# Performance work log

Hardware: AMD Instinct MI355X
Metric: run time of the kernel (lower is better)

Reference implementation:

```python
import jax, jax.numpy as jnp
import numpy as np

B, N, F_IN, F_OUT = 32, 1024, 256, 256
K_NEIGHBORS = 64
TEMPERATURE = 1.0
LN_EPS = 1e-5


def setup_inputs() -> dict:
    key = jax.random.key(0)
    ks = jax.random.split(key, 10)
    s_in = 1.0 / np.sqrt(F_IN)
    s_out = 1.0 / np.sqrt(F_OUT)
    # learned static adjacency: 0.1 everywhere + 0.9 on diagonal (self loops)
    static_edge_weights = jnp.full((N, N), 0.1, dtype=jnp.float32) + 0.9 * jnp.eye(N, dtype=jnp.float32)
    return {
        "x": jax.random.normal(ks[0], (B, N, F_IN), dtype=jnp.float32),
        "wq": jax.random.uniform(ks[1], (F_IN, F_OUT), jnp.float32, -s_in, s_in),
        "bq": jnp.zeros((F_OUT,), jnp.float32),
        "wk": jax.random.uniform(ks[2], (F_IN, F_OUT), jnp.float32, -s_in, s_in),
        "bk": jnp.zeros((F_OUT,), jnp.float32),
        "wv": jax.random.uniform(ks[3], (F_IN, F_OUT), jnp.float32, -s_in, s_in),
        "bv": jnp.zeros((F_OUT,), jnp.float32),
        "static_edge_weights": static_edge_weights,
        "w1": jax.random.uniform(ks[4], (F_OUT, F_OUT), jnp.float32, -s_out, s_out),
        "b1": jnp.zeros((F_OUT,), jnp.float32),
        "ln_g": jnp.ones((F_OUT,), jnp.float32),
        "ln_b": jnp.zeros((F_OUT,), jnp.float32),
        "w2": jax.random.uniform(ks[5], (F_OUT, F_OUT), jnp.float32, -s_out, s_out),
        "b2": jnp.zeros((F_OUT,), jnp.float32),
    }


def reference(x, wq, bq, wk, bk, wv, bv, static_edge_weights, w1, b1, ln_g, ln_b, w2, b2):
    Bc, Nc, _ = x.shape
    q = jnp.einsum("bnf,fo->bno", x, wq) + bq
    k = jnp.einsum("bnf,fo->bno", x, wk) + bk
    v = jnp.einsum("bnf,fo->bno", x, wv) + bv
    # [B, N, N] attention scores with learned static adjacency bias
    scores = jnp.einsum("bnd,bmd->bnm", q, k) / jnp.sqrt(jnp.float32(F_OUT))
    scores = scores + static_edge_weights[None, :, :]
    # top-k sparsification along last dim
    _, topk_idx = jax.lax.top_k(scores, K_NEIGHBORS)  # [B, N, K]
    bi = jnp.arange(Bc)[:, None, None]
    ni = jnp.arange(Nc)[None, :, None]
    mask = jnp.zeros(scores.shape, dtype=bool).at[bi, ni, topk_idx].set(True)
    scores = jnp.where(mask, scores, jnp.float32(-1e9))
    attn = jax.nn.softmax(scores / TEMPERATURE, axis=-1)
    messages = jnp.einsum("bnm,bmd->bnd", attn, v)
    # out_mlp: Linear -> LayerNorm -> ReLU -> Linear
    h = jnp.einsum("bnd,de->bne", messages, w1) + b1
    mu = jnp.mean(h, axis=-1, keepdims=True)
    var = jnp.mean(jnp.square(h - mu), axis=-1, keepdims=True)
    h = (h - mu) / jnp.sqrt(var + LN_EPS) * ln_g + ln_b
    h = jax.nn.relu(h)
    h = jnp.einsum("bnd,de->bne", h, w2) + b2
    out = h + v  # residual
    return (out, attn)
```

## Files before the change

### kernel.cpp

```cpp
#include <hip/hip_runtime.h>
#include <cstdint>

#define NB 32
#define NNODES 1024
#define DD 256
#define KNB 64
#define MTOT (NB * NNODES)

#define INV65536 1.52587890625e-05f
#define KCELL 2.44140625e-4f

typedef _Float16 half8 __attribute__((ext_vector_type(8)));
typedef _Float16 half4 __attribute__((ext_vector_type(4)));
typedef float f32x4 __attribute__((ext_vector_type(4)));

typedef __attribute__((address_space(3))) uint32_t lds_u32;
typedef __attribute__((address_space(1))) uint32_t glb_u32;

__device__ __forceinline__ void gll16(const _Float16* g, _Float16* l) {
  __builtin_amdgcn_global_load_lds((const glb_u32*)g, (lds_u32*)l, 16, 0, 0);
}

__device__ __forceinline__ void split2(float v, _Float16& h, _Float16& l) {
  h = (_Float16)v;
  l = (_Float16)(v - (float)h);
}

__global__ __launch_bounds__(256) void prep_w(const float* __restrict__ wq,
                                              const float* __restrict__ wk,
                                              const float* __restrict__ wv,
                                              const float* __restrict__ w1,
                                              const float* __restrict__ w2,
                                              _Float16* __restrict__ WT) {
  const int idx = blockIdx.x * 256 + threadIdx.x;
  const int wsel = idx >> 16;
  const int rem = idx & 65535;
  const int k = rem >> 8, n = rem & 255;
  const float* src = (wsel == 0) ? wq : (wsel == 1) ? wk : (wsel == 2) ? wv : (wsel == 3) ? w1 : w2;
  const float v = src[rem] * 1024.0f;
  _Float16 h1, h2;
  split2(v, h1, h2);
  WT[(size_t)wsel * 131072 + n * 256 + k] = h1;
  WT[(size_t)wsel * 131072 + 65536 + n * 256 + k] = h2;
}

__global__ __launch_bounds__(256) void prep_x(const float* __restrict__ x,
                                              _Float16* __restrict__ X1,
                                              _Float16* __restrict__ X2) {
  const size_t i = ((size_t)blockIdx.x * 256 + threadIdx.x) * 8;
  const float4 a = *(const float4*)(x + i);
  const float4 bb = *(const float4*)(x + i + 4);
  const float vals[8] = {a.x, a.y, a.z, a.w, bb.x, bb.y, bb.z, bb.w};
  half8 h, l;
#pragma unroll
  for (int e = 0; e < 8; ++e) {
    _Float16 hh, ll;
    split2(vals[e] * 64.0f, hh, ll);
    h[e] = hh;
    l[e] = ll;
  }
  *(half8*)(X1 + i) = h;
  *(half8*)(X2 + i) = l;
}

#define SWZ_OFF(r, cc) ((r) * 64 + (((cc) ^ ((r)&7)) << 3))

__global__ __launch_bounds__(256) void gemm_qkv(const _Float16* __restrict__ X1,
                                                const _Float16* __restrict__ X2,
                                                const _Float16* __restrict__ WT,
                                                const float* __restrict__ bq,
                                                const float* __restrict__ bk,
                                                const float* __restrict__ bv,
                                                _Float16* __restrict__ Q1, _Float16* __restrict__ Q2,
                                                _Float16* __restrict__ K1, _Float16* __restrict__ K2,
                                                float* __restrict__ V,
                                                _Float16* __restrict__ V16) {
  __shared__ _Float16 sm[4 * 8192];
  _Float16* sA1 = sm;
  _Float16* sA2 = sm + 8192;
  _Float16* sB1 = sm + 16384;
  _Float16* sB2 = sm + 24576;

  const int tid = threadIdx.x;
  const int lane = tid & 63, w = tid >> 6;
  const int r16 = lane & 15, kg = lane >> 4;
  const int rsub = lane >> 3, csub = lane & 7;
  const int wm = (w >> 1) * 64, wn = (w & 1) * 64;

  const int id = blockIdx.x;
  const int c8 = id & 7, t = id >> 3;
  const int gy = (t / 6) * 8 + c8;
  const int j6 = t % 6;
  const int wsel = j6 >> 1;
  const int n0 = (j6 & 1) * 128;
  const int m0 = gy * 128;
  const bool full = (wsel != 2);

  const _Float16* pB1 = WT + (size_t)wsel * 131072;
  const _Float16* pB2 = pB1 + 65536;

  f32x4 acc[4][4];
#pragma unroll
  for (int i = 0; i < 4; ++i)
#pragma unroll
    for (int j = 0; j < 4; ++j) acc[i][j] = f32x4{0.f, 0.f, 0.f, 0.f};

  for (int k0 = 0; k0 < DD; k0 += 64) {
    __syncthreads();
#pragma unroll
    for (int it = 0; it < 4; ++it) {
      const int r = (w << 5) + (it << 3) + rsub;
      const int swz = ((csub ^ (r & 7)) << 3);
      const int ldso = (w << 11) + (it << 9);
      gll16(X1 + (size_t)(m0 + r) * DD + k0 + swz, sA1 + ldso);
      gll16(pB1 + (size_t)(n0 + r) * DD + k0 + swz, sB1 + ldso);
      if (full) {
        gll16(X2 + (size_t)(m0 + r) * DD + k0 + swz, sA2 + ldso);
        gll16(pB2 + (size_t)(n0 + r) * DD + k0 + swz, sB2 + ldso);
      }
    }
    __syncthreads();

#pragma unroll
    for (int s = 0; s < 2; ++s) {
      half8 aA[4], aB[4], bA[4], bB[4];
#pragma unroll
      for (int mi = 0; mi < 4; ++mi) {
        const int off = SWZ_OFF(wm + mi * 16 + r16, s * 4 + kg);
        aA[mi] = *(const half8*)(sA1 + off);
      }
#pragma unroll
      for (int nj = 0; nj < 4; ++nj) {
        const int off = SWZ_OFF(wn + nj * 16 + r16, s * 4 + kg);
        bA[nj] = *(const half8*)(sB1 + off);
      }
      if (full) {
#pragma unroll
        for (int mi = 0; mi < 4; ++mi) {
          const int off = SWZ_OFF(wm + mi * 16 + r16, s * 4 + kg);
          aB[mi] = *(const half8*)(sA2 + off);
        }
#pragma unroll
        for (int nj = 0; nj < 4; ++nj) {
          const int off = SWZ_OFF(wn + nj * 16 + r16, s * 4 + kg);
          bB[nj] = *(const half8*)(sB2 + off);
        }
      }
#pragma unroll
      for (int mi = 0; mi < 4; ++mi)
#pragma unroll
        for (int nj = 0; nj < 4; ++nj) {
          acc[mi][nj] = __builtin_amdgcn_mfma_f32_16x16x32_f16(aA[mi], bA[nj], acc[mi][nj], 0, 0, 0);
          if (full) {
            acc[mi][nj] = __builtin_amdgcn_mfma_f32_16x16x32_f16(aA[mi], bB[nj], acc[mi][nj], 0, 0, 0);
            acc[mi][nj] = __builtin_amdgcn_mfma_f32_16x16x32_f16(aB[mi], bA[nj], acc[mi][nj], 0, 0, 0);
          }
        }
    }
  }

  const float* bsel = (wsel == 0) ? bq : (wsel == 1) ? bk : bv;
  _Float16* P1 = (wsel == 0) ? Q1 : K1;
  _Float16* P2 = (wsel == 0) ? Q2 : K2;
#pragma unroll
  for (int mi = 0; mi < 4; ++mi)
#pragma unroll
    for (int nj = 0; nj < 4; ++nj) {
      const int col = n0 + wn + nj * 16 + r16;
#pragma unroll
      for (int j = 0; j < 4; ++j) {
        const int rr = m0 + wm + mi * 16 + kg * 4 + j;
        if (wsel == 2) {
          const float val = acc[mi][nj][j] * INV65536 + bsel[col];
          V[(size_t)rr * DD + col] = val;
          if (V16) V16[(size_t)rr * DD + col] = (_Float16)val;
        } else {
          const float qv = acc[mi][nj][j] * (1.0f / 1024.0f) + 64.0f * bsel[col];
          _Float16 h1, h2;
          split2(qv, h1, h2);
          P1[(size_t)rr * DD + col] = h1;
          P2[(size_t)rr * DD + col] = h2;
        }
      }
    }
}

template <int EPI>
__global__ __launch_bounds__(256) void gemm_split(const _Float16* __restrict__ A1,
                                                  const _Float16* __restrict__ A2,
                                                  const _Float16* __restrict__ B1g,
                                                  const _Float16* __restrict__ B2g,
                                                  const float* __restrict__ bias,
                                                  const float* __restrict__ resid,
                                                  float* __restrict__ C) {
  __shared__ _Float16 sm[4 * 8192];
  _Float16* sA1 = sm;
  _Float16* sA2 = sm + 8192;
  _Float16* sB1 = sm + 16384;
  _Float16* sB2 = sm + 24576;

  const int tid = threadIdx.x;
  const int lane = tid & 63, w = tid >> 6;
  const int r16 = lane & 15, kg = lane >> 4;
  const int rsub = lane >> 3, csub = lane & 7;
  const int wm = (w >> 1) * 64, wn = (w & 1) * 64;

  const int n0 = blockIdx.x * 128;
  const int m0 = blockIdx.y * 128;

  const _Float16* pB1 = B1g;
  const _Float16* pB2 = B2g;
  if (EPI == 2) {
    const size_t boff = (size_t)(m0 >> 10) * NNODES * DD;
    pB1 += boff;
    pB2 += boff;
  }

  f32x4 acc[4][4];
#pragma unroll
  for (int i = 0; i < 4; ++i)
#pragma unroll
    for (int j = 0; j < 4; ++j) acc[i][j] = f32x4{0.f, 0.f, 0.f, 0.f};

  for (int k0 = 0; k0 < DD; k0 += 64) {
    __syncthreads();
#pragma unroll
    for (int it = 0; it < 4; ++it) {
      const int r = (w << 5) + (it << 3) + rsub;
      const int swz = ((csub ^ (r & 7)) << 3);
      const int ldso = (w << 11) + (it << 9);
      gll16(A1 + (size_t)(m0 + r) * DD + k0 + swz, sA1 + ldso);
      if (EPI == 2) gll16(A2 + (size_t)(m0 + r) * DD + k0 + swz, sA2 + ldso);
      gll16(pB1 + (size_t)(n0 + r) * DD + k0 + swz, sB1 + ldso);
      gll16(pB2 + (size_t)(n0 + r) * DD + k0 + swz, sB2 + ldso);
    }
    __syncthreads();

#pragma unroll
    for (int s = 0; s < 2; ++s) {
      half8 aA[4], aB[4], bA[4], bB[4];
#pragma unroll
      for (int mi = 0; mi < 4; ++mi) {
        const int off = SWZ_OFF(wm + mi * 16 + r16, s * 4 + kg);
        aA[mi] = *(const half8*)(sA1 + off);
        if (EPI == 2) aB[mi] = *(const half8*)(sA2 + off);
      }
#pragma unroll
      for (int nj = 0; nj < 4; ++nj) {
        const int off = SWZ_OFF(wn + nj * 16 + r16, s * 4 + kg);
        bA[nj] = *(const half8*)(sB1 + off);
        bB[nj] = *(const half8*)(sB2 + off);
      }
#pragma unroll
      for (int mi = 0; mi < 4; ++mi)
#pragma unroll
        for (int nj = 0; nj < 4; ++nj) {
          acc[mi][nj] = __builtin_amdgcn_mfma_f32_16x16x32_f16(aA[mi], bA[nj], acc[mi][nj], 0, 0, 0);
          acc[mi][nj] = __builtin_amdgcn_mfma_f32_16x16x32_f16(aA[mi], bB[nj], acc[mi][nj], 0, 0, 0);
          if (EPI == 2)
            acc[mi][nj] = __builtin_amdgcn_mfma_f32_16x16x32_f16(aB[mi], bA[nj], acc[mi][nj], 0, 0, 0);
        }
    }
  }

#pragma unroll
  for (int mi = 0; mi < 4; ++mi)
#pragma unroll
    for (int nj = 0; nj < 4; ++nj) {
      const int col = n0 + wn + nj * 16 + r16;
#pragma unroll
      for (int j = 0; j < 4; ++j) {
        const int rr = m0 + wm + mi * 16 + kg * 4 + j;
        const float v = acc[mi][nj][j] * INV65536;
        if (EPI == 2) {
          const float sv = v + bias[(size_t)(rr & (NNODES - 1)) * NNODES + col];
          const float f = fminf(fmaxf((sv + 8.0f) * 4096.0f, 0.0f), 65535.0f);
          uint16_t* kbase = (uint16_t*)((char*)C + (size_t)rr * 4096 + 2048);
          kbase[col] = (uint16_t)(unsigned)f;
        } else if (EPI == 0) {
          C[(size_t)rr * DD + col] = v + bias[col];
        } else {
          C[(size_t)rr * DD + col] = v + bias[col] + resid[(size_t)rr * DD + col];
        }
      }
    }
}

template <bool USE16>
__global__ __launch_bounds__(256) void topk_softmax_msg(float* __restrict__ S,
                                                        const float* __restrict__ V,
                                                        const _Float16* __restrict__ V16,
                                                        const _Float16* __restrict__ Q1,
                                                        const _Float16* __restrict__ Q2,
                                                        const _Float16* __restrict__ K1,
                                                        const _Float16* __restrict__ K2,
                                                        const float* __restrict__ adj,
                                                        _Float16* __restrict__ M1) {
  const int tid = threadIdx.x;
  const int w = tid >> 6, lane = tid & 63;
  const int id = blockIdx.x;
  const int xcd = id & 7, t = id >> 3;
  const int b = (t >> 8) * 8 + xcd;
  const int row = b * NNODES + (t & 255) * 4 + w;
  const int m = row & (NNODES - 1);
  float* Srow = S + (size_t)row * NNODES;
  const uint16_t* krow = (const uint16_t*)((const char*)S + (size_t)row * 4096 + 2048);

  __shared__ float2 spair[4][KNB];
  __shared__ int cidxs[4][32];
  __shared__ float cex[4][32];
  __shared__ int csel[4][32];

  if (lane < KNB) spair[w][lane] = make_float2(0.0f, __int_as_float(0));

  const uint4 u0 = *(const uint4*)(krow + lane * 8);
  const uint4 u1 = *(const uint4*)(krow + 512 + lane * 8);
  int k[16];
  {
    const unsigned uu[8] = {u0.x, u0.y, u0.z, u0.w, u1.x, u1.y, u1.z, u1.w};
#pragma unroll
    for (int q = 0; q < 8; ++q) {
      k[q * 2] = (int)(uu[q] & 0xffffu);
      k[q * 2 + 1] = (int)(uu[q] >> 16);
    }
  }

  float st[16];
#pragma unroll
  for (int t2 = 0; t2 < 16; ++t2) st[t2] = fmaf((float)k[t2] + 0.5f, KCELL, -8.0f);

  int cur = 0;
#pragma unroll 1
  for (int bit = 15; bit >= 0; --bit) {
    const int cand = cur | (1 << bit);
    int cnt = 0;
#pragma unroll
    for (int t2 = 0; t2 < 16; ++t2) cnt += (int)__popcll(__ballot(k[t2] >= cand));
    if (cnt >= KNB) cur = cand;
  }

  const int kHi = cur + 2;
  const int kLo = cur - 1;

  const unsigned long long ltmask = (1ull << lane) - 1ull;
  unsigned hm = 0u, cm = 0u;
  int cpos[16];
  int nhi = 0, ncand = 0;
#pragma unroll
  for (int g = 0; g < 2; ++g) {
    bool hiv[8], cdv[8];
    unsigned long long mh[8], mc[8];
#pragma unroll
    for (int e = 0; e < 8; ++e) {
      const int t2 = g * 8 + e;
      hiv[e] = (k[t2] >= kHi);
      cdv[e] = (!hiv[e]) && (k[t2] >= kLo);
      mh[e] = __ballot(hiv[e]);
      mc[e] = __ballot(cdv[e]);
    }
    int below = 0, tot_h = 0, tot_c = 0;
#pragma unroll
    for (int e = 0; e < 8; ++e) {
      below += (int)__popcll(mc[e] & ltmask);
      tot_h += (int)__popcll(mh[e]);
      tot_c += (int)__popcll(mc[e]);
    }
    int own = 0;
#pragma unroll
    for (int e = 0; e < 8; ++e) {
      const int t2 = g * 8 + e;
      cpos[t2] = -1;
      if (hiv[e]) hm |= (1u << t2);
      if (cdv[e]) {
        cm |= (1u << t2);
        const int p = ncand + below + own;
        cpos[t2] = p;
        if (p < 32) cidxs[w][p] = g * 512 + lane * 8 + e;
        ++own;
      }
    }
    nhi += tot_h;
    ncand += tot_c;
  }
  const int need = KNB - nhi;

  unsigned selm;
  if (ncand == need) {
    selm = hm | cm;
  } else {
    const int nc = (ncand <= 32) ? ncand : 32;
    const int nd = (need <= nc) ? need : nc;
    const size_t qoff = (size_t)row * DD + lane * 4;
    const half4 q1v = *(const half4*)(Q1 + qoff);
    const half4 q2v = *(const half4*)(Q2 + qoff);
    float qf[4];
#pragma unroll
    for (int e = 0; e < 4; ++e) qf[e] = (float)q1v[e] + (float)q2v[e];
    const float* adjrow = adj + (size_t)m * NNODES;
#pragma unroll 1
    for (int t2 = 0; t2 < nc; ++t2) {
      const int j = cidxs[w][t2];
      const size_t koff = ((size_t)b * NNODES + j) * DD + lane * 4;
      const half4 k1v = *(const half4*)(K1 + koff);
      const half4 k2v = *(const half4*)(K2 + koff);
      float part = 0.0f;
#pragma unroll
      for (int e = 0; e < 4; ++e) part = fmaf(qf[e], (float)k1v[e] + (float)k2v[e], part);
#pragma unroll
      for (int off = 32; off > 0; off >>= 1) part += __shfl_xor(part, off);
      if (lane == 0) cex[w][t2] = part * INV65536 + adjrow[j];
    }
    if (lane < nc) {
      const float et = cex[w][lane];
      int rank = 0;
      for (int u = 0; u < nc; ++u) {
        const float eu = cex[w][u];
        rank += (eu > et || (eu == et && u < lane)) ? 1 : 0;
      }
      csel[w][lane] = (rank < nd) ? 1 : 0;
    }
    selm = hm;
#pragma unroll
    for (int t2 = 0; t2 < 16; ++t2) {
      if (((cm >> t2) & 1u) && cpos[t2] >= 0 && cpos[t2] < 32 && csel[w][cpos[t2]]) selm |= (1u << t2);
    }
  }

  float rmax = st[0];
#pragma unroll
  for (int t2 = 1; t2 < 16; ++t2) rmax = fmaxf(rmax, st[t2]);
#pragma unroll
  for (int off = 32; off > 0; off >>= 1) rmax = fmaxf(rmax, __shfl_xor(rmax, off));

  float p[16];
  float sum = 0.0f;
#pragma unroll
  for (int t2 = 0; t2 < 16; ++t2) {
    p[t2] = __expf(st[t2] - rmax);
    if ((selm >> t2) & 1u) sum += p[t2];
  }
#pragma unroll
  for (int off = 32; off > 0; off >>= 1) sum += __shfl_xor(sum, off);
  const float inv = 1.0f / sum;

  int run = 0;
#pragma unroll
  for (int g = 0; g < 2; ++g) {
    bool sel8[8];
    unsigned long long ms[8];
#pragma unroll
    for (int e = 0; e < 8; ++e) {
      sel8[e] = (selm >> (g * 8 + e)) & 1u;
      ms[e] = __ballot(sel8[e]);
    }
    int below = 0, tot = 0;
#pragma unroll
    for (int e = 0; e < 8; ++e) {
      below += (int)__popcll(ms[e] & ltmask);
      tot += (int)__popcll(ms[e]);
    }
    float ow[8];
    int own = 0;
#pragma unroll
    for (int e = 0; e < 8; ++e) {
      const int t2 = g * 8 + e;
      const float aw = sel8[e] ? p[t2] * inv : 0.0f;
      ow[e] = aw;
      if (sel8[e]) {
        const int pos = run + below + own;
        if (pos < KNB) spair[w][pos] = make_float2(aw, __int_as_float(g * 512 + lane * 8 + e));
        ++own;
      }
    }
    float* dst = Srow + g * 512 + lane * 8;
    *(float4*)(dst) = make_float4(ow[0], ow[1], ow[2], ow[3]);
    *(float4*)(dst + 4) = make_float4(ow[4], ow[5], ow[6], ow[7]);
    run += tot;
  }

  float4 acc = {0.0f, 0.0f, 0.0f, 0.0f};
  if (USE16) {
    const _Float16* Vb = V16 + (size_t)b * NNODES * DD;
#pragma unroll 4
    for (int t2 = 0; t2 < KNB; ++t2) {
      const float2 pr = spair[w][t2];
      const int j = __float_as_int(pr.y);
      const half4 vv = *(const half4*)(Vb + (size_t)j * DD + lane * 4);
      acc.x = fmaf(pr.x, (float)vv[0], acc.x);
      acc.y = fmaf(pr.x, (float)vv[1], acc.y);
      acc.z = fmaf(pr.x, (float)vv[2], acc.z);
      acc.w = fmaf(pr.x, (float)vv[3], acc.w);
    }
  } else {
    const float* Vb = V + (size_t)b * NNODES * DD;
#pragma unroll 2
    for (int t2 = 0; t2 < KNB; ++t2) {
      const float2 pr = spair[w][t2];
      const int j = __float_as_int(pr.y);
      const float4 vv = *(const float4*)(Vb + (size_t)j * DD + lane * 4);
      acc.x = fmaf(pr.x, vv.x, acc.x);
      acc.y = fmaf(pr.x, vv.y, acc.y);
      acc.z = fmaf(pr.x, vv.z, acc.z);
      acc.w = fmaf(pr.x, vv.w, acc.w);
    }
  }
  half4 m1;
  m1[0] = (_Float16)(acc.x * 64.0f);
  m1[1] = (_Float16)(acc.y * 64.0f);
  m1[2] = (_Float16)(acc.z * 64.0f);
  m1[3] = (_Float16)(acc.w * 64.0f);
  *(half4*)(M1 + (size_t)row * DD + lane * 4) = m1;
}

__global__ __launch_bounds__(256) void ln_relu(const float* __restrict__ H,
                                               const float* __restrict__ g,
                                               const float* __restrict__ bta,
                                               _Float16* __restrict__ H1) {
  const int row = blockIdx.x;
  const int c = threadIdx.x;
  const int wv = c >> 6, ln = c & 63;
  const float h = H[(size_t)row * DD + c];

  __shared__ float part[4], part2[4];
  float v = h;
#pragma unroll
  for (int off = 32; off > 0; off >>= 1) v += __shfl_xor(v, off);
  if (ln == 0) part[wv] = v;
  __syncthreads();
  const float mu = (part[0] + part[1] + part[2] + part[3]) * (1.0f / 256.0f);

  const float d = h - mu;
  float sq = d * d;
#pragma unroll
  for (int off = 32; off > 0; off >>= 1) sq += __shfl_xor(sq, off);
  if (ln == 0) part2[wv] = sq;
  __syncthreads();
  const float var = (part2[0] + part2[1] + part2[2] + part2[3]) * (1.0f / 256.0f);

  const float y = fmaxf(d * (1.0f / sqrtf(var + 1e-5f)) * g[c] + bta[c], 0.0f);
  H1[(size_t)row * DD + c] = (_Float16)(y * 64.0f);
}

extern "C" void kernel_launch(void* const* d_in, const int* in_sizes, int n_in,
                              void* d_out, int out_size, void* d_ws, size_t ws_size,
                              hipStream_t stream) {
  (void)in_sizes; (void)n_in; (void)out_size;
  const float* x   = (const float*)d_in[0];
  const float* wq  = (const float*)d_in[1];
  const float* bq  = (const float*)d_in[2];
  const float* wk  = (const float*)d_in[3];
  const float* bk  = (const float*)d_in[4];
  const float* wv  = (const float*)d_in[5];
  const float* bv  = (const float*)d_in[6];
  const float* adj = (const float*)d_in[7];
  const float* w1  = (const float*)d_in[8];
  const float* b1  = (const float*)d_in[9];
  const float* lng = (const float*)d_in[10];
  const float* lnb = (const float*)d_in[11];
  const float* w2  = (const float*)d_in[12];
  const float* b2  = (const float*)d_in[13];

  const size_t BND = (size_t)MTOT * DD;
  float* outp  = (float*)d_out;
  float* attnp = outp + BND;
  float* V = outp;

  _Float16* X1 = (_Float16*)attnp;
  _Float16* X2 = X1 + BND;

  _Float16* Q1 = (_Float16*)d_ws;
  _Float16* Q2 = Q1 + BND;
  _Float16* K1 = Q2 + BND;
  _Float16* K2 = K1 + BND;
  _Float16* WT = K2 + BND;
  _Float16* V16p = WT + 5 * 131072;
  const size_t need16 = (size_t)(V16p + BND - (_Float16*)d_ws) * sizeof(_Float16);
  const bool use16 = (ws_size >= need16);
  _Float16* V16 = use16 ? V16p : nullptr;

  _Float16* M1 = Q1;
  float* H = (float*)K1;
  _Float16* H1 = Q1;

  const dim3 blk(256);

  prep_w<<<dim3(1280), blk, 0, stream>>>(wq, wk, wv, w1, w2, WT);
  prep_x<<<dim3(4096), blk, 0, stream>>>(x, X1, X2);
  gemm_qkv<<<dim3(1536), blk, 0, stream>>>(X1, X2, WT, bq, bk, bv, Q1, Q2, K1, K2, V, V16);
  gemm_split<2><<<dim3(8, 256), blk, 0, stream>>>(Q1, Q2, K1, K2, adj, nullptr, attnp);
  if (use16) {
    topk_softmax_msg<true><<<dim3(MTOT / 4), blk, 0, stream>>>(attnp, V, V16, Q1, Q2, K1, K2, adj, M1);
  } else {
    topk_softmax_msg<false><<<dim3(MTOT / 4), blk, 0, stream>>>(attnp, V, nullptr, Q1, Q2, K1, K2, adj, M1);
  }
  gemm_split<0><<<dim3(2, 256), blk, 0, stream>>>(M1, nullptr, WT + 3 * 131072,
                                                  WT + 3 * 131072 + 65536, b1, nullptr, H);
  ln_relu<<<dim3(MTOT), blk, 0, stream>>>(H, lng, lnb, H1);
  gemm_split<1><<<dim3(2, 256), blk, 0, stream>>>(H1, nullptr, WT + 4 * 131072,
                                                  WT + 4 * 131072 + 65536, b2, V, outp);
}
```

Measured before the change: 338.6 us.

## Drop fp32 V and Q low-part in score GEMM, widen top-k window

V is now stored only as fp16 and used both for message gathering and the residual, so the fp32 V write and its fallback path go away. The QK^T score GEMM drops the Q low-half split product, removing one third of its MFMAs and one A-tile load per stage. The top-k candidate window is widened to make up for the lower score precision, and gather offsets are precomputed as byte offsets. The kernel also gains a launch-bounds occupancy hint. The cost is lower accuracy in the scores and residual, plus more work in the refinement step.

```diff
diff --git a/kernel.cpp b/kernel.cpp
--- a/kernel.cpp
+++ b/kernel.cpp
@@ -73,7 +73,6 @@
                                                 const float* __restrict__ bv,
                                                 _Float16* __restrict__ Q1, _Float16* __restrict__ Q2,
                                                 _Float16* __restrict__ K1, _Float16* __restrict__ K2,
-                                                float* __restrict__ V,
                                                 _Float16* __restrict__ V16) {
   __shared__ _Float16 sm[4 * 8192];
   _Float16* sA1 = sm;
@@ -171,9 +170,7 @@
       for (int j = 0; j < 4; ++j) {
         const int rr = m0 + wm + mi * 16 + kg * 4 + j;
         if (wsel == 2) {
-          const float val = acc[mi][nj][j] * INV65536 + bsel[col];
-          V[(size_t)rr * DD + col] = val;
-          if (V16) V16[(size_t)rr * DD + col] = (_Float16)val;
+          V16[(size_t)rr * DD + col] = (_Float16)(acc[mi][nj][j] * INV65536 + bsel[col]);
         } else {
           const float qv = acc[mi][nj][j] * (1.0f / 1024.0f) + 64.0f * bsel[col];
           _Float16 h1, h2;
@@ -187,17 +184,15 @@
 
 template <int EPI>
 __global__ __launch_bounds__(256) void gemm_split(const _Float16* __restrict__ A1,
-                                                  const _Float16* __restrict__ A2,
                                                   const _Float16* __restrict__ B1g,
                                                   const _Float16* __restrict__ B2g,
                                                   const float* __restrict__ bias,
-                                                  const float* __restrict__ resid,
+                                                  const _Float16* __restrict__ resid16,
                                                   float* __restrict__ C) {
-  __shared__ _Float16 sm[4 * 8192];
+  __shared__ _Float16 sm[3 * 8192];
   _Float16* sA1 = sm;
-  _Float16* sA2 = sm + 8192;
-  _Float16* sB1 = sm + 16384;
-  _Float16* sB2 = sm + 24576;
+  _Float16* sB1 = sm + 8192;
+  _Float16* sB2 = sm + 16384;
 
   const int tid = threadIdx.x;
   const int lane = tid & 63, w = tid >> 6;
@@ -230,7 +225,6 @@
       const int swz = ((csub ^ (r & 7)) << 3);
       const int ldso = (w << 11) + (it << 9);
       gll16(A1 + (size_t)(m0 + r) * DD + k0 + swz, sA1 + ldso);
-      if (EPI == 2) gll16(A2 + (size_t)(m0 + r) * DD + k0 + swz, sA2 + ldso);
       gll16(pB1 + (size_t)(n0 + r) * DD + k0 + swz, sB1 + ldso);
       gll16(pB2 + (size_t)(n0 + r) * DD + k0 + swz, sB2 + ldso);
     }
@@ -238,12 +232,11 @@
 
 #pragma unroll
     for (int s = 0; s < 2; ++s) {
-      half8 aA[4], aB[4], bA[4], bB[4];
+      half8 aA[4], bA[4], bB[4];
 #pragma unroll
       for (int mi = 0; mi < 4; ++mi) {
         const int off = SWZ_OFF(wm + mi * 16 + r16, s * 4 + kg);
         aA[mi] = *(const half8*)(sA1 + off);
-        if (EPI == 2) aB[mi] = *(const half8*)(sA2 + off);
       }
 #pragma unroll
       for (int nj = 0; nj < 4; ++nj) {
@@ -257,8 +250,6 @@
         for (int nj = 0; nj < 4; ++nj) {
           acc[mi][nj] = __builtin_amdgcn_mfma_f32_16x16x32_f16(aA[mi], bA[nj], acc[mi][nj], 0, 0, 0);
           acc[mi][nj] = __builtin_amdgcn_mfma_f32_16x16x32_f16(aA[mi], bB[nj], acc[mi][nj], 0, 0, 0);
-          if (EPI == 2)
-            acc[mi][nj] = __builtin_amdgcn_mfma_f32_16x16x32_f16(aB[mi], bA[nj], acc[mi][nj], 0, 0, 0);
         }
     }
   }
@@ -280,22 +271,20 @@
         } else if (EPI == 0) {
           C[(size_t)rr * DD + col] = v + bias[col];
         } else {
-          C[(size_t)rr * DD + col] = v + bias[col] + resid[(size_t)rr * DD + col];
+          C[(size_t)rr * DD + col] = v + bias[col] + (float)resid16[(size_t)rr * DD + col];
         }
       }
     }
 }
 
-template <bool USE16>
-__global__ __launch_bounds__(256) void topk_softmax_msg(float* __restrict__ S,
-                                                        const float* __restrict__ V,
-                                                        const _Float16* __restrict__ V16,
-                                                        const _Float16* __restrict__ Q1,
-                                                        const _Float16* __restrict__ Q2,
-                                                        const _Float16* __restrict__ K1,
-                                                        const _Float16* __restrict__ K2,
-                                                        const float* __restrict__ adj,
-                                                        _Float16* __restrict__ M1) {
+__global__ __launch_bounds__(256, 4) void topk_softmax_msg(float* __restrict__ S,
+                                                           const _Float16* __restrict__ V16,
+                                                           const _Float16* __restrict__ Q1,
+                                                           const _Float16* __restrict__ Q2,
+                                                           const _Float16* __restrict__ K1,
+                                                           const _Float16* __restrict__ K2,
+                                                           const float* __restrict__ adj,
+                                                           _Float16* __restrict__ M1) {
   const int tid = threadIdx.x;
   const int w = tid >> 6, lane = tid & 63;
   const int id = blockIdx.x;
@@ -339,8 +328,8 @@
     if (cnt >= KNB) cur = cand;
   }
 
-  const int kHi = cur + 2;
-  const int kLo = cur - 1;
+  const int kHi = cur + 17;
+  const int kLo = cur - 16;
 
   const unsigned long long ltmask = (1ull << lane) - 1ull;
   unsigned hm = 0u, cm = 0u;
@@ -468,7 +457,8 @@
       ow[e] = aw;
       if (sel8[e]) {
         const int pos = run + below + own;
-        if (pos < KNB) spair[w][pos] = make_float2(aw, __int_as_float(g * 512 + lane * 8 + e));
+        if (pos < KNB)
+          spair[w][pos] = make_float2(aw, __int_as_float((g * 512 + lane * 8 + e) * (DD * 2)));
         ++own;
       }
     }
@@ -479,30 +469,16 @@
   }
 
   float4 acc = {0.0f, 0.0f, 0.0f, 0.0f};
-  if (USE16) {
-    const _Float16* Vb = V16 + (size_t)b * NNODES * DD;
+  const char* Vbase = (const char*)(V16 + (size_t)b * NNODES * DD) + lane * 8;
 #pragma unroll 4
-    for (int t2 = 0; t2 < KNB; ++t2) {
-      const float2 pr = spair[w][t2];
-      const int j = __float_as_int(pr.y);
-      const half4 vv = *(const half4*)(Vb + (size_t)j * DD + lane * 4);
-      acc.x = fmaf(pr.x, (float)vv[0], acc.x);
-      acc.y = fmaf(pr.x, (float)vv[1], acc.y);
-      acc.z = fmaf(pr.x, (float)vv[2], acc.z);
-      acc.w = fmaf(pr.x, (float)vv[3], acc.w);
-    }
-  } else {
-    const float* Vb = V + (size_t)b * NNODES * DD;
-#pragma unroll 2
-    for (int t2 = 0; t2 < KNB; ++t2) {
-      const float2 pr = spair[w][t2];
-      const int j = __float_as_int(pr.y);
-      const float4 vv = *(const float4*)(Vb + (size_t)j * DD + lane * 4);
-      acc.x = fmaf(pr.x, vv.x, acc.x);
-      acc.y = fmaf(pr.x, vv.y, acc.y);
-      acc.z = fmaf(pr.x, vv.z, acc.z);
-      acc.w = fmaf(pr.x, vv.w, acc.w);
-    }
+  for (int t2 = 0; t2 < KNB; ++t2) {
+    const float2 pr = spair[w][t2];
+    const int off = __float_as_int(pr.y);
+    const half4 vv = *(const half4*)(Vbase + off);
+    acc.x = fmaf(pr.x, (float)vv[0], acc.x);
+    acc.y = fmaf(pr.x, (float)vv[1], acc.y);
+    acc.z = fmaf(pr.x, (float)vv[2], acc.z);
+    acc.w = fmaf(pr.x, (float)vv[3], acc.w);
   }
   half4 m1;
   m1[0] = (_Float16)(acc.x * 64.0f);
@@ -544,7 +520,7 @@
 extern "C" void kernel_launch(void* const* d_in, const int* in_sizes, int n_in,
                               void* d_out, int out_size, void* d_ws, size_t ws_size,
                               hipStream_t stream) {
-  (void)in_sizes; (void)n_in; (void)out_size;
+  (void)in_sizes; (void)n_in; (void)out_size; (void)ws_size;
   const float* x   = (const float*)d_in[0];
   const float* wq  = (const float*)d_in[1];
   const float* bq  = (const float*)d_in[2];
@@ -563,7 +539,6 @@
   const size_t BND = (size_t)MTOT * DD;
   float* outp  = (float*)d_out;
   float* attnp = outp + BND;
-  float* V = outp;
 
   _Float16* X1 = (_Float16*)attnp;
   _Float16* X2 = X1 + BND;
@@ -573,10 +548,7 @@
   _Float16* K1 = Q2 + BND;
   _Float16* K2 = K1 + BND;
   _Float16* WT = K2 + BND;
-  _Float16* V16p = WT + 5 * 131072;
-  const size_t need16 = (size_t)(V16p + BND - (_Float16*)d_ws) * sizeof(_Float16);
-  const bool use16 = (ws_size >= need16);
-  _Float16* V16 = use16 ? V16p : nullptr;
+  _Float16* V16 = WT + 5 * 131072;
 
   _Float16* M1 = Q1;
   float* H = (float*)K1;
@@ -586,16 +558,12 @@
 
   prep_w<<<dim3(1280), blk, 0, stream>>>(wq, wk, wv, w1, w2, WT);
   prep_x<<<dim3(4096), blk, 0, stream>>>(x, X1, X2);
-  gemm_qkv<<<dim3(1536), blk, 0, stream>>>(X1, X2, WT, bq, bk, bv, Q1, Q2, K1, K2, V, V16);
-  gemm_split<2><<<dim3(8, 256), blk, 0, stream>>>(Q1, Q2, K1, K2, adj, nullptr, attnp);
-  if (use16) {
-    topk_softmax_msg<true><<<dim3(MTOT / 4), blk, 0, stream>>>(attnp, V, V16, Q1, Q2, K1, K2, adj, M1);
-  } else {
-    topk_softmax_msg<false><<<dim3(MTOT / 4), blk, 0, stream>>>(attnp, V, nullptr, Q1, Q2, K1, K2, adj, M1);
-  }
-  gemm_split<0><<<dim3(2, 256), blk, 0, stream>>>(M1, nullptr, WT + 3 * 131072,
-                                                  WT + 3 * 131072 + 65536, b1, nullptr, H);
+  gemm_qkv<<<dim3(1536), blk, 0, stream>>>(X1, X2, WT, bq, bk, bv, Q1, Q2, K1, K2, V16);
+  gemm_split<2><<<dim3(8, 256), blk, 0, stream>>>(Q1, K1, K2, adj, nullptr, attnp);
+  topk_softmax_msg<<<dim3(MTOT / 4), blk, 0, stream>>>(attnp, V16, Q1, Q2, K1, K2, adj, M1);
+  gemm_split<0><<<dim3(2, 256), blk, 0, stream>>>(M1, WT + 3 * 131072, WT + 3 * 131072 + 65536,
+                                                  b1, nullptr, H);
   ln_relu<<<dim3(MTOT), blk, 0, stream>>>(H, lng, lnb, H1);
-  gemm_split<1><<<dim3(2, 256), blk, 0, stream>>>(H1, nullptr, WT + 4 * 131072,
-                                                  WT + 4 * 131072 + 65536, b2, V, outp);
-}
+  gemm_split<1><<<dim3(2, 256), blk, 0, stream>>>(H1, WT + 4 * 131072, WT + 4 * 131072 + 65536,
+                                                  b2, V16, outp);
+}
```

Result: no change. 333.8 us (-1.4%).
